# Kernel tuning notes

Measured on AMD Instinct MI355X. Metric: run time of the kernel, lower is better.

## Reference

```python
import jax, jax.numpy as jnp
import numpy as np

B, S, D, H, EXP = 4, 4096, 1024, 8, 4
E = D // H            # per-head hidden dim = hidden_dim // heads
DC = S // 512         # decay_constant


def setup_inputs() -> dict:
    key = jax.random.key(0)
    ks = jax.random.split(key, 10)
    n = lambda k, shp, s: jax.random.normal(k, shp, dtype=jnp.float32) * s
    return {
        "x": n(ks[0], (B, S, D), 1.0),
        "ln1_g": jnp.ones((D,), jnp.float32),
        "ln1_b": jnp.zeros((D,), jnp.float32),
        "w1": n(ks[1], (EXP * D, D), 1.0 / np.sqrt(D).astype(np.float32)),
        "b1": jnp.zeros((EXP * D,), jnp.float32),
        "w2": n(ks[2], (D, EXP * D), 1.0 / np.sqrt(EXP * D).astype(np.float32)),
        "b2": jnp.zeros((D,), jnp.float32),
        "ln2_g": jnp.ones((D,), jnp.float32),
        "ln2_b": jnp.zeros((D,), jnp.float32),
        "proj_w": n(ks[3], (H, E, D), 1.0 / np.sqrt(D).astype(np.float32)),
        "proj_b": jnp.zeros((H, E), jnp.float32),
        # per-index scalar mixing weights; keep away from 0 (Col head divides by it)
        "mix_w": jax.random.uniform(ks[4], (H, S), jnp.float32, 0.5, 1.5),
        "mix_b": n(ks[5], (H, S), 0.02),
        "decay_raw": jax.random.uniform(ks[6], (H,), jnp.float32, 0.85, 1.05),
        "out_w": n(ks[7], (D, D), 1.0 / np.sqrt(D).astype(np.float32)),
        "out_b": jnp.zeros((D,), jnp.float32),
    }


def _ln(x, g, b):
    m = x.mean(-1, keepdims=True)
    v = x.var(-1, keepdims=True)
    return (x - m) / jnp.sqrt(v + 1e-5) * g + b


def reference(x, ln1_g, ln1_b, w1, b1, w2, b2, ln2_g, ln2_b,
              proj_w, proj_b, mix_w, mix_b, decay_raw, out_w, out_b):
    # --- channel mixing (per-token MLP with residual) ---
    res = x
    h = _ln(x, ln1_g, ln1_b)
    h = jnp.einsum('bsd,fd->bsf', h, w1) + b1
    h = jax.nn.silu(h)
    h = jnp.einsum('bsf,df->bsd', h, w2) + b2
    x = h + res

    # --- token mixing: MixedRepeatHeads, indices 0..S-1 as a decayed scan ---
    res = x
    h = _ln(x, ln2_g, ln2_b)
    p = jnp.einsum('bsd,hed->hbse', h, proj_w) + proj_b[:, None, None, :]  # [H,B,S,E]

    decay = jnp.clip(decay_raw, 0.9, 1.0) ** (1.0 / DC)  # [H]
    half = H // 2
    is_col = jnp.arange(H) < half  # first half Col heads, second half Row heads
    # Col: cache_t = p_t + d*cache;     out_t = w_t*cache_t + b_t
    # Row: cache_t = w_t*p_t + d*cache; out_t =     cache_t + b_t
    c1 = jnp.where(is_col[:, None], 1.0, mix_w)  # [H,S] pre-scan scale
    c2 = jnp.where(is_col[:, None], mix_w, 1.0)  # [H,S] post-scan scale

    u = p * c1[:, None, :, None]          # [H,B,S,E]
    u_t = jnp.moveaxis(u, 2, 0)           # [S,H,B,E] time-major

    def step(cache, xs):
        us, c2s, bs = xs                   # [H,B,E], [H], [H]
        cache = us + decay[:, None, None] * cache
        out = c2s[:, None, None] * cache + bs[:, None, None]
        return cache, out

    cache0 = jnp.zeros((H, B, E), x.dtype)
    _, outs = jax.lax.scan(step, cache0, (u_t, c2.T, mix_b.T))  # [S,H,B,E]

    mixed = jnp.transpose(outs, (2, 0, 1, 3)).reshape(B, S, D)  # concat heads
    mixed = jnp.einsum('bsd,fd->bsf', mixed, out_w) + out_b      # out_proj
    return mixed + res
```

## Files before the change

kernel.cpp:

```cpp
#include <hip/hip_runtime.h>
#include <math.h>

constexpr int B = 4, S = 4096, D = 1024, H = 8, EXPF = 4;
constexpr int E = D / H;
constexpr int F = EXPF * D;
constexpr int M = B * S;
constexpr int DC = S / 512;
constexpr int FC = 2048;
constexpr int L = 64;
constexpr int NCHUNK = S / L;
constexpr int NCH = H * B * E;

typedef _Float16 f16;
typedef f16  h8  __attribute__((ext_vector_type(8)));
typedef f16  h4  __attribute__((ext_vector_type(4)));
typedef float fx4 __attribute__((ext_vector_type(4)));

__device__ __forceinline__ void gld16(const f16* g, f16* l) {
    __builtin_amdgcn_global_load_lds(
        (const __attribute__((address_space(1))) unsigned int*)g,
        (__attribute__((address_space(3))) unsigned int*)l, 16, 0, 0);
}

__global__ __launch_bounds__(256) void cvt_f16(const float* __restrict__ src,
                                               f16* __restrict__ dst, int n) {
    const int stride = gridDim.x * blockDim.x * 8;
    for (int i = (blockIdx.x * blockDim.x + threadIdx.x) * 8; i < n; i += stride) {
        const float4 a = *(const float4*)(src + i);
        const float4 b = *(const float4*)(src + i + 4);
        h8 o;
        o[0] = (f16)a.x; o[1] = (f16)a.y; o[2] = (f16)a.z; o[3] = (f16)a.w;
        o[4] = (f16)b.x; o[5] = (f16)b.y; o[6] = (f16)b.z; o[7] = (f16)b.w;
        *(h8*)(dst + i) = o;
    }
}

__global__ __launch_bounds__(256) void ln_f16(const float* __restrict__ x,
                                              const float* __restrict__ g,
                                              const float* __restrict__ b,
                                              f16* __restrict__ out) {
    const int row = blockIdx.x;
    const int t = threadIdx.x;
    const float4 v = ((const float4*)(x + (size_t)row * D))[t];
    float s  = v.x + v.y + v.z + v.w;
    float ss = v.x * v.x + v.y * v.y + v.z * v.z + v.w * v.w;
#pragma unroll
    for (int off = 32; off; off >>= 1) {
        s  += __shfl_xor(s, off, 64);
        ss += __shfl_xor(ss, off, 64);
    }
    __shared__ float sm[8];
    const int wave = t >> 6, lane = t & 63;
    if (lane == 0) { sm[wave] = s; sm[4 + wave] = ss; }
    __syncthreads();
    s  = sm[0] + sm[1] + sm[2] + sm[3];
    ss = sm[4] + sm[5] + sm[6] + sm[7];
    const float mean = s * (1.0f / D);
    const float var  = ss * (1.0f / D) - mean * mean;
    const float inv  = rsqrtf(var + 1e-5f);
    const float4 gg = ((const float4*)g)[t];
    const float4 bb = ((const float4*)b)[t];
    h4 o;
    o[0] = (f16)((v.x - mean) * inv * gg.x + bb.x);
    o[1] = (f16)((v.y - mean) * inv * gg.y + bb.y);
    o[2] = (f16)((v.z - mean) * inv * gg.z + bb.z);
    o[3] = (f16)((v.w - mean) * inv * gg.w + bb.w);
    *(h4*)(out + (size_t)row * D + t * 4) = o;
}

#define BAR  __builtin_amdgcn_s_barrier()
#define LGK0 asm volatile("s_waitcnt lgkmcnt(0)" ::: "memory")
#define VMC4 asm volatile("s_waitcnt vmcnt(4)" ::: "memory")
#define VMC2 asm volatile("s_waitcnt vmcnt(2)" ::: "memory")
#define VMC0 asm volatile("s_waitcnt vmcnt(0)" ::: "memory")

template <int EPI>
__global__ __launch_bounds__(512, 2) void hgemm256(const f16* __restrict__ A,
                                                   const f16* __restrict__ W,
                                                   const float* __restrict__ bias,
                                                   const float* res,
                                                   void* Cv,
                                                   int K, int lda, int ldw, int N) {
    __shared__ __align__(16) char lds[131072];
    const int t = threadIdx.x;
    const int wid = t >> 6, lane = t & 63;
    const int wr = wid >> 2, wc = wid & 3;
    const int l16 = lane & 15, kg = lane >> 4;
    const int bn = blockIdx.x, bm = blockIdx.y;
    const int nh = wc >> 1;

    const int kx0 = (kg << 4) ^ ((l16 & 7) << 4);
    const int kx1 = kx0 ^ 64;
    const int arow = (wr * 64 + l16) * 128;
    const int brow = ((wc & 1) * 64 + l16) * 128;
    const int rsub = lane >> 3;
    const int kf   = ((lane & 7) ^ rsub) << 3;
    const f16* Abase = A + (size_t)(bm * 256 + wid * 8 + rsub) * lda + kf;
    const f16* Bbase = W + (size_t)(bn * 256 + wid * 8 + rsub) * ldw + kf;

#define STAGE_A(DB, MH, KT) do { \
        const f16* g_ = Abase + (size_t)(MH) * 64 * lda + (size_t)(KT) * 64; \
        f16* d_ = (f16*)(lds + ((DB) * 2 + (MH)) * 16384 + wid * 1024); \
        gld16(g_, d_); gld16(g_ + (size_t)128 * lda, d_ + 4096); \
    } while (0)
#define STAGE_B(DB, NH, KT) do { \
        const f16* g_ = Bbase + (size_t)(NH) * 128 * ldw + (size_t)(KT) * 64; \
        f16* d_ = (f16*)(lds + 65536 + ((DB) * 2 + (NH)) * 16384 + wid * 1024); \
        gld16(g_, d_); gld16(g_ + (size_t)64 * ldw, d_ + 4096); \
    } while (0)
#define READ_A(DB, MH) do { \
        const char* r_ = lds + ((DB) * 2 + (MH)) * 16384 + arow; \
        _Pragma("unroll") for (int mf = 0; mf < 4; ++mf) { \
            af[mf][0] = *(const h8*)(r_ + mf * 2048 + kx0); \
            af[mf][1] = *(const h8*)(r_ + mf * 2048 + kx1); } \
    } while (0)
#define READ_B(DB, NG) do { \
        const char* r_ = lds + 65536 + ((DB) * 2 + nh) * 16384 + brow; \
        _Pragma("unroll") for (int nf = 0; nf < 2; ++nf) { \
            bf[(NG) * 2 + nf][0] = *(const h8*)(r_ + ((NG) * 2 + nf) * 2048 + kx0); \
            bf[(NG) * 2 + nf][1] = *(const h8*)(r_ + ((NG) * 2 + nf) * 2048 + kx1); } \
    } while (0)
#define MMA(MH, NG) do { \
        __builtin_amdgcn_s_setprio(1); \
        _Pragma("unroll") for (int nf = 0; nf < 2; ++nf) \
        _Pragma("unroll") for (int mf = 0; mf < 4; ++mf) \
        _Pragma("unroll") for (int kk = 0; kk < 2; ++kk) \
            acc[(MH) * 4 + mf][(NG) * 2 + nf] = __builtin_amdgcn_mfma_f32_16x16x32_f16( \
                af[mf][kk], bf[(NG) * 2 + nf][kk], acc[(MH) * 4 + mf][(NG) * 2 + nf], 0, 0, 0); \
        __builtin_amdgcn_s_setprio(0); \
    } while (0)

    fx4 acc[8][4] = {};
    h8 af[4][2], bf[4][2];

    STAGE_A(0, 0, 0); STAGE_A(0, 1, 0); STAGE_B(0, 0, 0); STAGE_B(0, 1, 0);
    STAGE_A(1, 0, 1);
    VMC2;
    BAR;

    const int NI = K >> 7;
    for (int i = 0; i < NI; ++i) {
        const int t1 = 2 * i + 1, n0 = 2 * i + 2, n1 = 2 * i + 3;
        const bool more = (i + 1 < NI);
        READ_A(0, 0); READ_B(0, 0);
        STAGE_A(1, 1, t1);
        BAR; LGK0; MMA(0, 0); BAR;
        READ_B(0, 1);
        STAGE_B(1, 0, t1); STAGE_B(1, 1, t1);
        BAR; LGK0; MMA(0, 1); BAR;
        READ_A(0, 1);
        if (more) STAGE_A(0, 0, n0);
        BAR; LGK0; MMA(1, 0); BAR;
        if (more) STAGE_B(0, 0, n0);
        BAR; MMA(1, 1);
        if (more) { VMC4; } else { VMC0; }
        BAR;
        READ_A(1, 0); READ_B(1, 0);
        if (more) STAGE_A(0, 1, n0);
        BAR; LGK0; MMA(0, 0); BAR;
        READ_B(1, 1);
        if (more) STAGE_B(0, 1, n0);
        BAR; LGK0; MMA(0, 1); BAR;
        READ_A(1, 1);
        BAR; LGK0; MMA(1, 0); BAR;
        if (more) STAGE_A(1, 0, n1);
        BAR; MMA(1, 1); VMC2; BAR;
    }

    const int rbase = bm * 256 + wr * 128;
    const int cbase = bn * 256 + wc * 64;
#pragma unroll
    for (int mf = 0; mf < 8; ++mf) {
#pragma unroll
        for (int nf = 0; nf < 4; ++nf) {
            const int col = cbase + nf * 16 + l16;
            float bv = 0.0f;
            if (EPI != 3) bv = bias[col];
#pragma unroll
            for (int j = 0; j < 4; ++j) {
                const int row = rbase + mf * 16 + kg * 4 + j;
                const size_t off = (size_t)row * N + col;
                float v = acc[mf][nf][j];
                if (EPI == 3) {
                    ((float*)Cv)[off] += v;
                } else {
                    v += bv;
                    if (EPI == 1) v = v / (1.0f + expf(-v));
                    if (EPI == 2) ((float*)Cv)[off] = v + res[off];
                    else          ((f16*)Cv)[off] = (f16)v;
                }
            }
        }
    }
#undef STAGE_A
#undef STAGE_B
#undef READ_A
#undef READ_B
#undef MMA
}

__device__ inline float head_decay(const float* decay_raw, int h) {
    const float dr = fminf(fmaxf(decay_raw[h], 0.9f), 1.0f);
    return powf(dr, 1.0f / (float)DC);
}

__global__ __launch_bounds__(256) void scan_carry(const f16* __restrict__ p,
                                                  const float* __restrict__ mix_w,
                                                  const float* __restrict__ decay_raw,
                                                  float* __restrict__ carry) {
    const int g = blockIdx.x * blockDim.x + threadIdx.x;
    const int e = g & (E - 1);
    const int chunk = (g >> 7) & (NCHUNK - 1);
    const int hb = g >> 13;
    const int h = hb >> 2, b = hb & 3;
    const float d = head_decay(decay_raw, h);
    const bool is_col = h < (H / 2);
    const int s0 = chunk * L;
    const f16* pp = p + ((size_t)(b * S + s0)) * D + h * E + e;
    const float* mw = mix_w + h * S + s0;
    float c = 0.0f;
#pragma unroll 4
    for (int i = 0; i < L; ++i) {
        float u = (float)pp[(size_t)i * D];
        if (!is_col) u *= mw[i];
        c = fmaf(d, c, u);
    }
    carry[chunk * NCH + hb * E + e] = c;
}

__global__ __launch_bounds__(256) void scan_prefix(const float* __restrict__ carry,
                                                   const float* __restrict__ decay_raw,
                                                   float* __restrict__ carry_in) {
    const int ch = blockIdx.x * blockDim.x + threadIdx.x;
    const int h = ch >> 9;
    const float d = head_decay(decay_raw, h);
    const float dL = powf(d, (float)L);
    float c = 0.0f;
    for (int j = 0; j < NCHUNK; ++j) {
        carry_in[j * NCH + ch] = c;
        c = fmaf(dL, c, carry[j * NCH + ch]);
    }
}

__global__ __launch_bounds__(256) void scan_apply(const f16* __restrict__ p,
                                                  const float* __restrict__ mix_w,
                                                  const float* __restrict__ mix_b,
                                                  const float* __restrict__ decay_raw,
                                                  const float* __restrict__ carry_in,
                                                  f16* __restrict__ mixed) {
    const int g = blockIdx.x * blockDim.x + threadIdx.x;
    const int e = g & (E - 1);
    const int chunk = (g >> 7) & (NCHUNK - 1);
    const int hb = g >> 13;
    const int h = hb >> 2, b = hb & 3;
    const float d = head_decay(decay_raw, h);
    const bool is_col = h < (H / 2);
    const int s0 = chunk * L;
    const f16* pp = p + ((size_t)(b * S + s0)) * D + h * E + e;
    f16* mo = mixed + ((size_t)(b * S + s0)) * D + h * E + e;
    const float* mw = mix_w + h * S + s0;
    const float* mb = mix_b + h * S + s0;
    float c = carry_in[chunk * NCH + hb * E + e];
#pragma unroll 4
    for (int i = 0; i < L; ++i) {
        const float w = mw[i];
        float u = (float)pp[(size_t)i * D];
        if (!is_col) u *= w;
        c = fmaf(d, c, u);
        float o = is_col ? fmaf(w, c, mb[i]) : (c + mb[i]);
        mo[(size_t)i * D] = (f16)o;
    }
}

extern "C" void kernel_launch(void* const* d_in, const int* in_sizes, int n_in,
                              void* d_out, int out_size, void* d_ws, size_t ws_size,
                              hipStream_t stream) {
    (void)in_sizes; (void)n_in; (void)out_size; (void)ws_size;
    const float* x         = (const float*)d_in[0];
    const float* ln1_g     = (const float*)d_in[1];
    const float* ln1_b     = (const float*)d_in[2];
    const float* w1        = (const float*)d_in[3];
    const float* b1        = (const float*)d_in[4];
    const float* w2        = (const float*)d_in[5];
    const float* b2        = (const float*)d_in[6];
    const float* ln2_g     = (const float*)d_in[7];
    const float* ln2_b     = (const float*)d_in[8];
    const float* proj_w    = (const float*)d_in[9];
    const float* proj_b    = (const float*)d_in[10];
    const float* mix_w     = (const float*)d_in[11];
    const float* mix_b     = (const float*)d_in[12];
    const float* decay_raw = (const float*)d_in[13];
    const float* out_w     = (const float*)d_in[14];
    const float* out_b     = (const float*)d_in[15];
    float* out = (float*)d_out;

    f16* lnbuf = (f16*)d_ws;
    f16* actc  = lnbuf + (size_t)M * D;
    f16* w1f   = actc + (size_t)M * FC;
    f16* w2f   = w1f + (size_t)F * D;
    f16* pjf   = w2f + (size_t)D * F;
    f16* owf   = pjf + (size_t)D * D;
    float* carry    = (float*)(owf + (size_t)D * D);
    float* carry_in = carry + (size_t)NCHUNK * NCH;
    f16* p     = actc;
    f16* mixed = lnbuf;
    float* x2  = out;

    const dim3 gD(D / 256, M / 256);
    const dim3 gC(FC / 256, M / 256);

    cvt_f16<<<1024, 256, 0, stream>>>(w1, w1f, F * D);
    cvt_f16<<<1024, 256, 0, stream>>>(w2, w2f, D * F);
    cvt_f16<<<256, 256, 0, stream>>>(proj_w, pjf, D * D);
    cvt_f16<<<256, 256, 0, stream>>>(out_w, owf, D * D);
    ln_f16<<<M, 256, 0, stream>>>(x, ln1_g, ln1_b, lnbuf);
    hgemm256<1><<<gC, 512, 0, stream>>>(lnbuf, w1f, b1, nullptr, actc, D, D, D, FC);
    hgemm256<2><<<gD, 512, 0, stream>>>(actc, w2f, b2, x, x2, FC, FC, F, D);
    hgemm256<1><<<gC, 512, 0, stream>>>(lnbuf, w1f + (size_t)FC * D, b1 + FC, nullptr, actc, D, D, D, FC);
    hgemm256<3><<<gD, 512, 0, stream>>>(actc, w2f + FC, nullptr, nullptr, x2, FC, FC, F, D);
    ln_f16<<<M, 256, 0, stream>>>(x2, ln2_g, ln2_b, lnbuf);
    hgemm256<0><<<gD, 512, 0, stream>>>(lnbuf, pjf, proj_b, nullptr, p, D, D, D, D);
    scan_carry <<<(NCH * NCHUNK) / 256, 256, 0, stream>>>(p, mix_w, decay_raw, carry);
    scan_prefix<<<NCH / 256, 256, 0, stream>>>(carry, decay_raw, carry_in);
    scan_apply <<<(NCH * NCHUNK) / 256, 256, 0, stream>>>(p, mix_w, mix_b, decay_raw,
                                                          carry_in, mixed);
    hgemm256<2><<<gD, 512, 0, stream>>>(mixed, owf, out_b, x2, out, D, D, D, D);
}
```

Measured before the change: 719.7 us.

## Merge weight conversions, remap GEMM tiles across XCDs, run FFN unchunked when workspace allows

Replaces the four weight-conversion launches with one combined kernel. Remaps the GEMM block index so that consecutive tiles land on the same XCD, which is meant to improve L2 reuse on MI355X's eight-XCD layout. If the workspace is large enough, the first MLP runs as one full-width up-projection and one full-K down-projection instead of two FC-sized chunks, which cuts launches and the extra read-modify-write of x2. The full-width path needs a much larger activation buffer and otherwise falls back to the chunked path.

```diff
diff --git a/kernel.cpp b/kernel.cpp
--- a/kernel.cpp
+++ b/kernel.cpp
@@ -22,16 +22,25 @@
         (__attribute__((address_space(3))) unsigned int*)l, 16, 0, 0);
 }
 
-__global__ __launch_bounds__(256) void cvt_f16(const float* __restrict__ src,
-                                               f16* __restrict__ dst, int n) {
-    const int stride = gridDim.x * blockDim.x * 8;
-    for (int i = (blockIdx.x * blockDim.x + threadIdx.x) * 8; i < n; i += stride) {
-        const float4 a = *(const float4*)(src + i);
-        const float4 b = *(const float4*)(src + i + 4);
+__global__ __launch_bounds__(256) void cvt_all(const float* __restrict__ s0, f16* __restrict__ d0, int n0,
+                                               const float* __restrict__ s1, f16* __restrict__ d1, int n1,
+                                               const float* __restrict__ s2, f16* __restrict__ d2, int n2,
+                                               const float* __restrict__ s3, f16* __restrict__ d3, int n3) {
+    const int total = (n0 + n1 + n2 + n3) / 8;
+    const int stride = gridDim.x * blockDim.x;
+    for (int c = blockIdx.x * blockDim.x + threadIdx.x; c < total; c += stride) {
+        int i = c * 8;
+        const float* s; f16* d;
+        if (i < n0)                { s = s0 + i;               d = d0 + i; }
+        else if (i < n0 + n1)      { s = s1 + (i - n0);        d = d1 + (i - n0); }
+        else if (i < n0 + n1 + n2) { s = s2 + (i - n0 - n1);   d = d2 + (i - n0 - n1); }
+        else                       { s = s3 + (i - n0 - n1 - n2); d = d3 + (i - n0 - n1 - n2); }
+        const float4 a = *(const float4*)s;
+        const float4 b = *(const float4*)(s + 4);
         h8 o;
         o[0] = (f16)a.x; o[1] = (f16)a.y; o[2] = (f16)a.z; o[3] = (f16)a.w;
         o[4] = (f16)b.x; o[5] = (f16)b.y; o[6] = (f16)b.z; o[7] = (f16)b.w;
-        *(h8*)(dst + i) = o;
+        *(h8*)d = o;
     }
 }
 
@@ -86,7 +95,11 @@
     const int wid = t >> 6, lane = t & 63;
     const int wr = wid >> 2, wc = wid & 3;
     const int l16 = lane & 15, kg = lane >> 4;
-    const int bn = blockIdx.x, bm = blockIdx.y;
+    const int nwg = gridDim.x * gridDim.y;
+    const int d   = blockIdx.y * gridDim.x + blockIdx.x;
+    const int cpx = nwg >> 3;
+    const int Lw  = (d & 7) * cpx + (d >> 3);
+    const int bn  = Lw % gridDim.x, bm = Lw / gridDim.x;
     const int nh = wc >> 1;
 
     const int kx0 = (kg << 4) ^ ((l16 & 7) << 4);
@@ -275,7 +288,7 @@
 extern "C" void kernel_launch(void* const* d_in, const int* in_sizes, int n_in,
                               void* d_out, int out_size, void* d_ws, size_t ws_size,
                               hipStream_t stream) {
-    (void)in_sizes; (void)n_in; (void)out_size; (void)ws_size;
+    (void)in_sizes; (void)n_in; (void)out_size;
     const float* x         = (const float*)d_in[0];
     const float* ln1_g     = (const float*)d_in[1];
     const float* ln1_b     = (const float*)d_in[2];
@@ -293,36 +306,66 @@
     const float* out_w     = (const float*)d_in[14];
     const float* out_b     = (const float*)d_in[15];
     float* out = (float*)d_out;
-
-    f16* lnbuf = (f16*)d_ws;
-    f16* actc  = lnbuf + (size_t)M * D;
-    f16* w1f   = actc + (size_t)M * FC;
-    f16* w2f   = w1f + (size_t)F * D;
-    f16* pjf   = w2f + (size_t)D * F;
-    f16* owf   = pjf + (size_t)D * D;
-    float* carry    = (float*)(owf + (size_t)D * D);
-    float* carry_in = carry + (size_t)NCHUNK * NCH;
-    f16* p     = actc;
-    f16* mixed = lnbuf;
     float* x2  = out;
 
+    const size_t FULL_WS = (size_t)M * D * 2 + (size_t)M * F * 2 +
+                           (size_t)F * D * 4 + (size_t)D * D * 4 +
+                           (size_t)NCHUNK * NCH * 8;
+
     const dim3 gD(D / 256, M / 256);
-    const dim3 gC(FC / 256, M / 256);
-
-    cvt_f16<<<1024, 256, 0, stream>>>(w1, w1f, F * D);
-    cvt_f16<<<1024, 256, 0, stream>>>(w2, w2f, D * F);
-    cvt_f16<<<256, 256, 0, stream>>>(proj_w, pjf, D * D);
-    cvt_f16<<<256, 256, 0, stream>>>(out_w, owf, D * D);
-    ln_f16<<<M, 256, 0, stream>>>(x, ln1_g, ln1_b, lnbuf);
-    hgemm256<1><<<gC, 512, 0, stream>>>(lnbuf, w1f, b1, nullptr, actc, D, D, D, FC);
-    hgemm256<2><<<gD, 512, 0, stream>>>(actc, w2f, b2, x, x2, FC, FC, F, D);
-    hgemm256<1><<<gC, 512, 0, stream>>>(lnbuf, w1f + (size_t)FC * D, b1 + FC, nullptr, actc, D, D, D, FC);
-    hgemm256<3><<<gD, 512, 0, stream>>>(actc, w2f + FC, nullptr, nullptr, x2, FC, FC, F, D);
-    ln_f16<<<M, 256, 0, stream>>>(x2, ln2_g, ln2_b, lnbuf);
-    hgemm256<0><<<gD, 512, 0, stream>>>(lnbuf, pjf, proj_b, nullptr, p, D, D, D, D);
-    scan_carry <<<(NCH * NCHUNK) / 256, 256, 0, stream>>>(p, mix_w, decay_raw, carry);
-    scan_prefix<<<NCH / 256, 256, 0, stream>>>(carry, decay_raw, carry_in);
-    scan_apply <<<(NCH * NCHUNK) / 256, 256, 0, stream>>>(p, mix_w, mix_b, decay_raw,
-                                                          carry_in, mixed);
-    hgemm256<2><<<gD, 512, 0, stream>>>(mixed, owf, out_b, x2, out, D, D, D, D);
-}
+
+    if (ws_size >= FULL_WS) {
+        f16* lnbuf = (f16*)d_ws;
+        f16* act   = lnbuf + (size_t)M * D;
+        f16* w1f   = act + (size_t)M * F;
+        f16* w2f   = w1f + (size_t)F * D;
+        f16* pjf   = w2f + (size_t)D * F;
+        f16* owf   = pjf + (size_t)D * D;
+        float* carry    = (float*)(owf + (size_t)D * D);
+        float* carry_in = carry + (size_t)NCHUNK * NCH;
+        f16* p     = act;
+        f16* mixed = lnbuf;
+
+        cvt_all<<<2048, 256, 0, stream>>>(w1, w1f, F * D, w2, w2f, D * F,
+                                          proj_w, pjf, D * D, out_w, owf, D * D);
+        ln_f16<<<M, 256, 0, stream>>>(x, ln1_g, ln1_b, lnbuf);
+        hgemm256<1><<<dim3(F / 256, M / 256), 512, 0, stream>>>(
+            lnbuf, w1f, b1, nullptr, act, D, D, D, F);
+        hgemm256<2><<<gD, 512, 0, stream>>>(act, w2f, b2, x, x2, F, F, F, D);
+        ln_f16<<<M, 256, 0, stream>>>(x2, ln2_g, ln2_b, lnbuf);
+        hgemm256<0><<<gD, 512, 0, stream>>>(lnbuf, pjf, proj_b, nullptr, p, D, D, D, D);
+        scan_carry <<<(NCH * NCHUNK) / 256, 256, 0, stream>>>(p, mix_w, decay_raw, carry);
+        scan_prefix<<<NCH / 256, 256, 0, stream>>>(carry, decay_raw, carry_in);
+        scan_apply <<<(NCH * NCHUNK) / 256, 256, 0, stream>>>(p, mix_w, mix_b, decay_raw,
+                                                              carry_in, mixed);
+        hgemm256<2><<<gD, 512, 0, stream>>>(mixed, owf, out_b, x2, out, D, D, D, D);
+    } else {
+        f16* lnbuf = (f16*)d_ws;
+        f16* actc  = lnbuf + (size_t)M * D;
+        f16* w1f   = actc + (size_t)M * FC;
+        f16* w2f   = w1f + (size_t)F * D;
+        f16* pjf   = w2f + (size_t)D * F;
+        f16* owf   = pjf + (size_t)D * D;
+        float* carry    = (float*)(owf + (size_t)D * D);
+        float* carry_in = carry + (size_t)NCHUNK * NCH;
+        f16* p     = actc;
+        f16* mixed = lnbuf;
+        const dim3 gC(FC / 256, M / 256);
+
+        cvt_all<<<2048, 256, 0, stream>>>(w1, w1f, F * D, w2, w2f, D * F,
+                                          proj_w, pjf, D * D, out_w, owf, D * D);
+        ln_f16<<<M, 256, 0, stream>>>(x, ln1_g, ln1_b, lnbuf);
+        hgemm256<1><<<gC, 512, 0, stream>>>(lnbuf, w1f, b1, nullptr, actc, D, D, D, FC);
+        hgemm256<2><<<gD, 512, 0, stream>>>(actc, w2f, b2, x, x2, FC, FC, F, D);
+        hgemm256<1><<<gC, 512, 0, stream>>>(lnbuf, w1f + (size_t)FC * D, b1 + FC,
+                                            nullptr, actc, D, D, D, FC);
+        hgemm256<3><<<gD, 512, 0, stream>>>(actc, w2f + FC, nullptr, nullptr, x2, FC, FC, F, D);
+        ln_f16<<<M, 256, 0, stream>>>(x2, ln2_g, ln2_b, lnbuf);
+        hgemm256<0><<<gD, 512, 0, stream>>>(lnbuf, pjf, proj_b, nullptr, p, D, D, D, D);
+        scan_carry <<<(NCH * NCHUNK) / 256, 256, 0, stream>>>(p, mix_w, decay_raw, carry);
+        scan_prefix<<<NCH / 256, 256, 0, stream>>>(carry, decay_raw, carry_in);
+        scan_apply <<<(NCH * NCHUNK) / 256, 256, 0, stream>>>(p, mix_w, mix_b, decay_raw,
+                                                              carry_in, mixed);
+        hgemm256<2><<<gD, 512, 0, stream>>>(mixed, owf, out_b, x2, out, D, D, D, D);
+    }
+}
```

Measured after the change: 680.9 us. 5.4% less time.
